# Kernel optimization log

Measured on AMD Instinct MI355X. Metric: run time of the kernel, lower is better.

The kernel has to match this reference:

```python
import jax, jax.numpy as jnp
import numpy as np

N = 100000        # nodes
E = 1600000       # edges (before self-loops)
IN_CH = 256       # input features
HEADS = 8         # conv1 heads; per-head dim also 8 (GATConv(in, heads, heads=heads))
HID = 8
NCLASS = 64
SLOPE = 0.2       # PyG leaky_relu negative slope


def _gat_conv(x, edge_index, W, att_src, att_dst, bias, heads, ch, concat):
    """PyG GATConv (eval mode): gather -> leaky_relu score -> segment softmax -> scatter."""
    n = x.shape[0]
    src, dst = edge_index[0], edge_index[1]
    h = (x @ W).reshape(n, heads, ch)                      # [N, H, C]
    a_src = jnp.einsum('nhc,hc->nh', h, att_src)           # [N, H]
    a_dst = jnp.einsum('nhc,hc->nh', h, att_dst)
    alpha = jax.nn.leaky_relu(a_src[src] + a_dst[dst], SLOPE)  # [E, H]
    # segment softmax over destination node
    amax = jax.ops.segment_max(alpha, dst, num_segments=n)     # [N, H]
    ex = jnp.exp(alpha - amax[dst])
    denom = jax.ops.segment_sum(ex, dst, num_segments=n)
    coef = ex / (denom[dst] + 1e-16)                           # [E, H]
    out = jax.ops.segment_sum(coef[:, :, None] * h[src], dst, num_segments=n)  # [N, H, C]
    if concat:
        out = out.reshape(n, heads * ch)
    else:
        out = out.mean(axis=1)
    return out + bias


def _add_self_loops(edge_index, n):
    loop = jnp.arange(n, dtype=edge_index.dtype)
    return jnp.concatenate([edge_index, jnp.stack([loop, loop])], axis=1)


def setup_inputs() -> dict:
    key = jax.random.key(0)
    ks = jax.random.split(key, 10)
    g = lambda k, shp, s: (jax.random.normal(k, shp, jnp.float32) * s)
    return {
        'x': jax.random.normal(ks[0], (N, IN_CH), jnp.float32),
        'edge_index': jax.random.randint(ks[1], (2, E), 0, N, dtype=jnp.int64),
        'W1': g(ks[2], (IN_CH, HEADS * HID), 1.0 / np.sqrt(IN_CH)),
        'att_src1': g(ks[3], (HEADS, HID), 0.3),
        'att_dst1': g(ks[4], (HEADS, HID), 0.3),
        'b1': jnp.zeros((HEADS * HID,), jnp.float32),
        'W2': g(ks[5], (HEADS * HID, NCLASS), 1.0 / np.sqrt(HEADS * HID)),
        'att_src2': g(ks[6], (1, NCLASS), 0.3),
        'att_dst2': g(ks[7], (1, NCLASS), 0.3),
        'b2': jnp.zeros((NCLASS,), jnp.float32),
    }


def reference(x, edge_index, W1, att_src1, att_dst1, b1, W2, att_src2, att_dst2, b2):
    ei = _add_self_loops(edge_index, x.shape[0])
    h = jax.nn.elu(_gat_conv(x, ei, W1, att_src1, att_dst1, b1, HEADS, HID, True))
    # dropout is a no-op in eval mode
    h = _gat_conv(h, ei, W2, att_src2, att_dst2, b2, 1, NCLASS, False)
    return jax.nn.log_softmax(h, axis=-1)
```

## Files before the change

kernel.cpp:

```cpp
#include <hip/hip_runtime.h>
#include <hip/hip_bf16.h>

#define LRELU_SLOPE 0.2f
#define CH2 6144
#define NBUK 256
#define BCAP 9728

typedef unsigned int uint;
typedef unsigned short ushort;
typedef short bt8 __attribute__((ext_vector_type(8)));
typedef float fx4 __attribute__((ext_vector_type(4)));

__device__ __forceinline__ float lrelu(float a) {
    return a > 0.f ? a : LRELU_SLOPE * a;
}
__device__ __forceinline__ ushort f2bf(float f) {
    uint u = __float_as_uint(f);
    return (ushort)((u + 0x7FFF + ((u >> 16) & 1)) >> 16);
}
__device__ __forceinline__ float bf2f(ushort h) {
    return __uint_as_float(((uint)h) << 16);
}

__global__ __launch_bounds__(256) void prep_wt(
    const float* __restrict__ W1, const float* __restrict__ W2,
    ushort* __restrict__ WT1, ushort* __restrict__ WT2)
{
    int idx = blockIdx.x * 256 + threadIdx.x;
    if (idx < 64 * 256) {
        int c = idx >> 8, k = idx & 255;
        WT1[idx] = f2bf(W1[k * 64 + c]);
    }
    int i2 = idx - 64 * 256;
    if (i2 >= 0 && i2 < 64 * 64) {
        int c = i2 >> 6, k = i2 & 63;
        WT2[i2] = f2bf(W2[k * 64 + c]);
    }
}

template<int K, bool INF32>
__global__ __launch_bounds__(256) void gemm_mfma(
    const void* __restrict__ Xv, const ushort* __restrict__ WT,
    ushort* __restrict__ OUT, int nrows)
{
    constexpr int LDW = K + 8;
    __shared__ ushort wt_l[64 * LDW];
    __shared__ ushort a_l[64 * 40];
    const int t = threadIdx.x;
    const int base = blockIdx.x * 64;

    for (int idx = t * 8; idx < 64 * K; idx += 256 * 8) {
        int r = idx / K, c = idx % K;
        *(uint4*)&wt_l[r * LDW + c] = *(const uint4*)&WT[idx];
    }
    __syncthreads();

    const int w = t >> 6, l = t & 63;
    const int frow = l & 15;
    const int kof = (l >> 4) * 8;
    fx4 acc[4] = {};

    for (int k0 = 0; k0 < K; k0 += 32) {
        if constexpr (INF32) {
            const float* X = (const float*)Xv;
            #pragma unroll
            for (int half = 0; half < 2; ++half) {
                int r = (t >> 3) + 32 * half;
                int kq = (t & 7) * 4;
                int gr = base + r;
                float4 v = make_float4(0.f, 0.f, 0.f, 0.f);
                if (gr < nrows) v = *(const float4*)(X + (size_t)gr * K + k0 + kq);
                ushort4 o;
                o.x = f2bf(v.x); o.y = f2bf(v.y); o.z = f2bf(v.z); o.w = f2bf(v.w);
                *(ushort4*)&a_l[r * 40 + kq] = o;
            }
        } else {
            const ushort* X = (const ushort*)Xv;
            int r = t >> 2;
            int kq = (t & 3) * 8;
            int gr = base + r;
            uint4 v = make_uint4(0, 0, 0, 0);
            if (gr < nrows) v = *(const uint4*)(X + (size_t)gr * K + k0 + kq);
            *(uint4*)&a_l[r * 40 + kq] = v;
        }
        __syncthreads();
        bt8 af = *(const bt8*)&a_l[(16 * w + frow) * 40 + kof];
        #pragma unroll
        for (int g = 0; g < 4; ++g) {
            bt8 bf = *(const bt8*)&wt_l[(16 * g + frow) * LDW + k0 + kof];
            acc[g] = __builtin_amdgcn_mfma_f32_16x16x32_bf16(af, bf, acc[g], 0, 0, 0);
        }
        __syncthreads();
    }

    const int orow0 = base + 16 * w + (l >> 4) * 4;
    const int ocol = l & 15;
    #pragma unroll
    for (int g = 0; g < 4; ++g) {
        #pragma unroll
        for (int r4 = 0; r4 < 4; ++r4) {
            int gr = orow0 + r4;
            if (gr < nrows) OUT[(size_t)gr * 64 + 16 * g + ocol] = f2bf(acc[g][r4]);
        }
    }
}

__global__ __launch_bounds__(256) void node_att_h8(
    const ushort* __restrict__ H, const float* __restrict__ att_s,
    const float* __restrict__ att_d,
    float* __restrict__ a_src, float* __restrict__ a_dst, int n)
{
    int node = blockIdx.x * 4 + (threadIdx.x >> 6);
    if (node >= n) return;
    int lane = threadIdx.x & 63;
    float h = bf2f(H[(size_t)node * 64 + lane]);
    float ps = h * att_s[lane];
    float pd = h * att_d[lane];
    #pragma unroll
    for (int off = 1; off < 8; off <<= 1) {
        ps += __shfl_xor(ps, off, 64);
        pd += __shfl_xor(pd, off, 64);
    }
    if ((lane & 7) == 0) {
        a_src[(size_t)node * 8 + (lane >> 3)] = ps;
        a_dst[(size_t)node * 8 + (lane >> 3)] = pd;
    }
}

__global__ __launch_bounds__(256) void node_att_h1(
    const ushort* __restrict__ H, const float* __restrict__ att_s,
    const float* __restrict__ att_d,
    float* __restrict__ a_src, float* __restrict__ a_dst, int n)
{
    int node = blockIdx.x * 4 + (threadIdx.x >> 6);
    if (node >= n) return;
    int lane = threadIdx.x & 63;
    float h = bf2f(H[(size_t)node * 64 + lane]);
    float ps = h * att_s[lane];
    float pd = h * att_d[lane];
    #pragma unroll
    for (int off = 1; off < 64; off <<= 1) {
        ps += __shfl_xor(ps, off, 64);
        pd += __shfl_xor(pd, off, 64);
    }
    if (lane == 0) { a_src[node] = ps; a_dst[node] = pd; }
}

__global__ void init_pcur(int* __restrict__ pcur)
{
    int t = threadIdx.x;
    if (t < NBUK) pcur[t] = t * BCAP;
}

__global__ __launch_bounds__(1024) void partition_pairs(
    const int* __restrict__ ei, int E_, int ET,
    int* __restrict__ pcur, uint* __restrict__ pairs)
{
    __shared__ int lcnt[NBUK], lsc[NBUK], lplace[NBUK], gpos[NBUK];
    const int t = threadIdx.x;
    const int base = blockIdx.x * CH2;
    const int total = min(CH2, ET - base);
    if (total <= 0) return;

    if (t < NBUK) lcnt[t] = 0;
    __syncthreads();

    uint pp[6]; int pk[6];
    #pragma unroll
    for (int i = 0; i < 6; ++i) {
        int idx = t + i * 1024;
        pk[i] = -1;
        if (idx < total) {
            int e = base + idx;
            int s, d;
            if (e < E_) { s = ei[e]; d = ei[E_ + e]; } else { s = d = e - E_; }
            pk[i] = d >> 9;
            pp[i] = (uint)s | ((uint)(d & 511) << 17);
            atomicAdd(&lcnt[pk[i]], 1);
        }
    }
    __syncthreads();

    if (t < NBUK) lsc[t] = lcnt[t];
    __syncthreads();
    for (int off = 1; off < NBUK; off <<= 1) {
        int add = 0;
        if (t < NBUK && t >= off) add = lsc[t - off];
        __syncthreads();
        if (t < NBUK) lsc[t] += add;
        __syncthreads();
    }
    if (t < NBUK) {
        int excl = lsc[t] - lcnt[t];
        lplace[t] = excl;
        int c = lcnt[t];
        gpos[t] = c ? (atomicAdd(&pcur[t], c) - excl) : 0;
    }
    __syncthreads();

    #pragma unroll
    for (int i = 0; i < 6; ++i) {
        if (pk[i] >= 0) {
            int slot = atomicAdd(&lplace[pk[i]], 1);
            pairs[gpos[pk[i]] + slot] = pp[i];
        }
    }
}

__global__ __launch_bounds__(256) void bucket_scan(
    const int* __restrict__ pcur, int* __restrict__ boff, int nbuk_used)
{
    __shared__ int sm[NBUK];
    int t = threadIdx.x;
    int v = (t < nbuk_used) ? (pcur[t] - t * BCAP) : 0;
    sm[t] = v; __syncthreads();
    for (int off = 1; off < NBUK; off <<= 1) {
        int add = (t >= off) ? sm[t - off] : 0;
        __syncthreads();
        sm[t] += add;
        __syncthreads();
    }
    boff[t] = sm[t] - v;
}

__global__ __launch_bounds__(1024) void phase2_build(
    const uint* __restrict__ pairs, const int* __restrict__ pcur,
    const int* __restrict__ boff,
    int* __restrict__ rp, int* __restrict__ ssrc, int n)
{
    __shared__ int hist[512], cur[512];
    const int k = blockIdx.x;
    const int t = threadIdx.x;
    const int beg = k * BCAP;
    const int cnt = pcur[k] - beg;
    const int bbase = boff[k];
    const int dbase = k << 9;

    if (t < 512) hist[t] = 0;
    __syncthreads();

    uint pp[10];
    int m = 0;
    for (int i = t; i < cnt; i += 1024) {
        uint p = pairs[beg + i];
        pp[m++] = p;
        atomicAdd(&hist[p >> 17], 1);
    }
    __syncthreads();

    int c0 = (t < 512) ? hist[t] : 0;
    for (int off = 1; off < 512; off <<= 1) {
        int add = 0;
        if (t < 512 && t >= off) add = hist[t - off];
        __syncthreads();
        if (t < 512) hist[t] += add;
        __syncthreads();
    }
    if (t < 512) {
        int node = dbase + t;
        if (node < n) rp[node] = bbase + hist[t];
        cur[t] = hist[t] - c0;
    }
    __syncthreads();

    m = 0;
    for (int i = t; i < cnt; i += 1024) {
        uint p = pp[m++];
        int j = p >> 17;
        int pos = bbase + atomicAdd(&cur[j], 1);
        ssrc[pos] = (int)(p & 0x1FFFF);
    }
}

__global__ __launch_bounds__(256) void gather_h8(
    const int* __restrict__ rp, const int* __restrict__ ssrc,
    const float* __restrict__ a_src, const float* __restrict__ a_dst,
    const ushort* __restrict__ HB, const float* __restrict__ bias,
    ushort* __restrict__ HACT, int n)
{
    int node = blockIdx.x * 8 + (threadIdx.x >> 5);
    if (node >= n) return;
    int hl = threadIdx.x & 31;
    int q = hl >> 2;
    int end = rp[node];
    int start = node ? rp[node - 1] : 0;
    float adh = a_dst[(size_t)node * 8 + q];
    float accx = 0.f, accy = 0.f, dsum = 0.f;

    for (int i0 = start; i0 < end; i0 += 32) {
        int cnt = min(32, end - i0);
        int sv = (hl < cnt) ? ssrc[i0 + hl] : 0;
        int j = 0;
        for (; j + 4 <= cnt; j += 4) {
            #pragma unroll
            for (int k = 0; k < 4; ++k) {
                int sj = __shfl(sv, j + k, 32);
                float a = a_src[(size_t)sj * 8 + q] + adh;
                a = a > 0.f ? a : LRELU_SLOPE * a;
                float e = __expf(a);
                uint hv = *(const uint*)(HB + (size_t)sj * 64 + hl * 2);
                dsum += e;
                accx += e * bf2f((ushort)(hv & 0xffff));
                accy += e * bf2f((ushort)(hv >> 16));
            }
        }
        for (; j < cnt; ++j) {
            int sj = __shfl(sv, j, 32);
            float a = a_src[(size_t)sj * 8 + q] + adh;
            a = a > 0.f ? a : LRELU_SLOPE * a;
            float e = __expf(a);
            uint hv = *(const uint*)(HB + (size_t)sj * 64 + hl * 2);
            dsum += e;
            accx += e * bf2f((ushort)(hv & 0xffff));
            accy += e * bf2f((ushort)(hv >> 16));
        }
    }
    float inv = 1.f / (dsum + 1e-16f);
    float2 bb = *(const float2*)(bias + hl * 2);
    float vx = accx * inv + bb.x;
    float vy = accy * inv + bb.y;
    vx = vx > 0.f ? vx : expm1f(vx);
    vy = vy > 0.f ? vy : expm1f(vy);
    uint pv = (uint)f2bf(vx) | ((uint)f2bf(vy) << 16);
    *(uint*)(HACT + (size_t)node * 64 + hl * 2) = pv;
}

__global__ __launch_bounds__(256) void gather_h1_lsm(
    const int* __restrict__ rp, const int* __restrict__ ssrc,
    const float* __restrict__ a_src, const float* __restrict__ a_dst,
    const ushort* __restrict__ HB, const float* __restrict__ bias,
    float* __restrict__ OUT, int n)
{
    int node = blockIdx.x * 8 + (threadIdx.x >> 5);
    if (node >= n) return;
    int hl = threadIdx.x & 31;
    int end = rp[node];
    int start = node ? rp[node - 1] : 0;
    float ad = a_dst[node];
    float accx = 0.f, accy = 0.f, dsum = 0.f;

    for (int i0 = start; i0 < end; i0 += 32) {
        int cnt = min(32, end - i0);
        int sv = (hl < cnt) ? ssrc[i0 + hl] : 0;
        int j = 0;
        for (; j + 4 <= cnt; j += 4) {
            #pragma unroll
            for (int k = 0; k < 4; ++k) {
                int sj = __shfl(sv, j + k, 32);
                float a = a_src[sj] + ad;
                a = a > 0.f ? a : LRELU_SLOPE * a;
                float e = __expf(a);
                uint hv = *(const uint*)(HB + (size_t)sj * 64 + hl * 2);
                dsum += e;
                accx += e * bf2f((ushort)(hv & 0xffff));
                accy += e * bf2f((ushort)(hv >> 16));
            }
        }
        for (; j < cnt; ++j) {
            int sj = __shfl(sv, j, 32);
            float a = a_src[sj] + ad;
            a = a > 0.f ? a : LRELU_SLOPE * a;
            float e = __expf(a);
            uint hv = *(const uint*)(HB + (size_t)sj * 64 + hl * 2);
            dsum += e;
            accx += e * bf2f((ushort)(hv & 0xffff));
            accy += e * bf2f((ushort)(hv >> 16));
        }
    }
    float inv = 1.f / (dsum + 1e-16f);
    float2 bb = *(const float2*)(bias + hl * 2);
    float vx = accx * inv + bb.x;
    float vy = accy * inv + bb.y;

    float m = fmaxf(vx, vy);
    #pragma unroll
    for (int off = 1; off < 32; off <<= 1) m = fmaxf(m, __shfl_xor(m, off, 32));
    float s = __expf(vx - m) + __expf(vy - m);
    #pragma unroll
    for (int off = 1; off < 32; off <<= 1) s += __shfl_xor(s, off, 32);
    float lse = m + __logf(s);
    *(float2*)(OUT + (size_t)node * 64 + hl * 2) = make_float2(vx - lse, vy - lse);
}

extern "C" void kernel_launch(void* const* d_in, const int* in_sizes, int n_in,
                              void* d_out, int out_size, void* d_ws, size_t ws_size,
                              hipStream_t stream)
{
    const float* x    = (const float*)d_in[0];
    const int*   ei   = (const int*)d_in[1];
    const float* W1   = (const float*)d_in[2];
    const float* as1w = (const float*)d_in[3];
    const float* ad1w = (const float*)d_in[4];
    const float* b1   = (const float*)d_in[5];
    const float* W2   = (const float*)d_in[6];
    const float* as2w = (const float*)d_in[7];
    const float* ad2w = (const float*)d_in[8];
    const float* b2   = (const float*)d_in[9];
    float* out = (float*)d_out;

    const int n  = in_sizes[0] / 256;
    const int E_ = in_sizes[1] / 2;
    const int ET = E_ + n;
    const int NBUKU = (n + 511) >> 9;

    char* wsb = (char*)d_ws;
    ushort* HACT = (ushort*)wsb;
    uint*   pairs= (uint*)wsb;
    ushort* HB   = HACT + (size_t)n * 64;
    float*  a_s1 = (float*)(HB + (size_t)n * 64);
    float*  a_d1 = a_s1 + (size_t)n * 8;
    float*  a_s2 = a_d1 + (size_t)n * 8;
    float*  a_d2 = a_s2 + n;
    int*    rp   = (int*)(a_d2 + n);
    int*    pcur = rp + n;
    int*    boff = pcur + NBUK;
    int*    ssrc = boff + NBUK;
    ushort* WT1  = (ushort*)(ssrc + ET);
    ushort* WT2  = WT1 + 64 * 256;

    const int gemm_grid = (n + 63) / 64;
    const int natt_grid = (n + 3) / 4;
    const int gath_grid = (n + 7) / 8;
    const int part_grid = (ET + CH2 - 1) / CH2;

    prep_wt<<<80, 256, 0, stream>>>(W1, W2, WT1, WT2);
    init_pcur<<<1, NBUK, 0, stream>>>(pcur);
    partition_pairs<<<part_grid, 1024, 0, stream>>>(ei, E_, ET, pcur, pairs);
    bucket_scan<<<1, NBUK, 0, stream>>>(pcur, boff, NBUKU);
    phase2_build<<<NBUKU, 1024, 0, stream>>>(pairs, pcur, boff, rp, ssrc, n);

    gemm_mfma<256, true><<<gemm_grid, 256, 0, stream>>>(x, WT1, HB, n);
    node_att_h8<<<natt_grid, 256, 0, stream>>>(HB, as1w, ad1w, a_s1, a_d1, n);
    gather_h8<<<gath_grid, 256, 0, stream>>>(rp, ssrc, a_s1, a_d1, HB, b1, HACT, n);

    gemm_mfma<64, false><<<gemm_grid, 256, 0, stream>>>(HACT, WT2, HB, n);
    node_att_h1<<<natt_grid, 256, 0, stream>>>(HB, as2w, ad2w, a_s2, a_d2, n);
    gather_h1_lsm<<<gath_grid, 256, 0, stream>>>(rp, ssrc, a_s2, a_d2, HB, b2, out, n);
}
```

Measured before the change: 198.1 us.

## Gather with 8 lanes per node using 16-byte vector loads; drop register cache in build

Both gather kernels now give each destination node 8 lanes instead of 32. Each lane loads 16 bytes (8 bf16 channels) per edge and processes the edges in fixed batches of 8, masking the tail. The log-softmax reduction shrinks to an 8-lane shuffle plus in-register work. This is meant to cut shuffle and instruction overhead per edge and widen memory transactions, but gives fewer lanes per edge and some wasted masked work on low-degree nodes. Separately, phase2_build re-reads pairs from global memory instead of caching them in a register array, which lowers register pressure at the cost of a second read.

```diff
diff --git a/kernel.cpp b/kernel.cpp
--- a/kernel.cpp
+++ b/kernel.cpp
@@ -239,13 +239,8 @@
     if (t < 512) hist[t] = 0;
     __syncthreads();
 
-    uint pp[10];
-    int m = 0;
-    for (int i = t; i < cnt; i += 1024) {
-        uint p = pairs[beg + i];
-        pp[m++] = p;
-        atomicAdd(&hist[p >> 17], 1);
-    }
+    for (int i = t; i < cnt; i += 1024)
+        atomicAdd(&hist[pairs[beg + i] >> 17], 1);
     __syncthreads();
 
     int c0 = (t < 512) ? hist[t] : 0;
@@ -263,9 +258,8 @@
     }
     __syncthreads();
 
-    m = 0;
     for (int i = t; i < cnt; i += 1024) {
-        uint p = pp[m++];
+        uint p = pairs[beg + i];
         int j = p >> 17;
         int pos = bbase + atomicAdd(&cur[j], 1);
         ssrc[pos] = (int)(p & 0x1FFFF);
@@ -278,51 +272,53 @@
     const ushort* __restrict__ HB, const float* __restrict__ bias,
     ushort* __restrict__ HACT, int n)
 {
-    int node = blockIdx.x * 8 + (threadIdx.x >> 5);
+    int node = blockIdx.x * 32 + (threadIdx.x >> 3);
     if (node >= n) return;
-    int hl = threadIdx.x & 31;
-    int q = hl >> 2;
+    int ol = threadIdx.x & 7;
     int end = rp[node];
     int start = node ? rp[node - 1] : 0;
-    float adh = a_dst[(size_t)node * 8 + q];
-    float accx = 0.f, accy = 0.f, dsum = 0.f;
-
-    for (int i0 = start; i0 < end; i0 += 32) {
-        int cnt = min(32, end - i0);
-        int sv = (hl < cnt) ? ssrc[i0 + hl] : 0;
-        int j = 0;
-        for (; j + 4 <= cnt; j += 4) {
-            #pragma unroll
-            for (int k = 0; k < 4; ++k) {
-                int sj = __shfl(sv, j + k, 32);
-                float a = a_src[(size_t)sj * 8 + q] + adh;
-                a = a > 0.f ? a : LRELU_SLOPE * a;
-                float e = __expf(a);
-                uint hv = *(const uint*)(HB + (size_t)sj * 64 + hl * 2);
-                dsum += e;
-                accx += e * bf2f((ushort)(hv & 0xffff));
-                accy += e * bf2f((ushort)(hv >> 16));
-            }
-        }
-        for (; j < cnt; ++j) {
-            int sj = __shfl(sv, j, 32);
-            float a = a_src[(size_t)sj * 8 + q] + adh;
+    float adh = a_dst[(size_t)node * 8 + ol];
+    float acc[8] = {};
+    float dsum = 0.f;
+
+    for (int i0 = start; i0 < end; i0 += 8) {
+        int cnt = min(8, end - i0);
+        int sv = (ol < cnt) ? ssrc[i0 + ol] : 0;
+        #pragma unroll
+        for (int j = 0; j < 8; ++j) {
+            int sj = __shfl(sv, j, 8);
+            float a = a_src[(size_t)sj * 8 + ol] + adh;
             a = a > 0.f ? a : LRELU_SLOPE * a;
             float e = __expf(a);
-            uint hv = *(const uint*)(HB + (size_t)sj * 64 + hl * 2);
+            e = (j < cnt) ? e : 0.f;
             dsum += e;
-            accx += e * bf2f((ushort)(hv & 0xffff));
-            accy += e * bf2f((ushort)(hv >> 16));
+            uint4 hv = *(const uint4*)(HB + (size_t)sj * 64 + ol * 8);
+            acc[0] += e * bf2f((ushort)(hv.x & 0xffff));
+            acc[1] += e * bf2f((ushort)(hv.x >> 16));
+            acc[2] += e * bf2f((ushort)(hv.y & 0xffff));
+            acc[3] += e * bf2f((ushort)(hv.y >> 16));
+            acc[4] += e * bf2f((ushort)(hv.z & 0xffff));
+            acc[5] += e * bf2f((ushort)(hv.z >> 16));
+            acc[6] += e * bf2f((ushort)(hv.w & 0xffff));
+            acc[7] += e * bf2f((ushort)(hv.w >> 16));
         }
     }
     float inv = 1.f / (dsum + 1e-16f);
-    float2 bb = *(const float2*)(bias + hl * 2);
-    float vx = accx * inv + bb.x;
-    float vy = accy * inv + bb.y;
-    vx = vx > 0.f ? vx : expm1f(vx);
-    vy = vy > 0.f ? vy : expm1f(vy);
-    uint pv = (uint)f2bf(vx) | ((uint)f2bf(vy) << 16);
-    *(uint*)(HACT + (size_t)node * 64 + hl * 2) = pv;
+    float4 b0 = *(const float4*)(bias + ol * 8);
+    float4 b1 = *(const float4*)(bias + ol * 8 + 4);
+    float v[8];
+    v[0] = acc[0] * inv + b0.x; v[1] = acc[1] * inv + b0.y;
+    v[2] = acc[2] * inv + b0.z; v[3] = acc[3] * inv + b0.w;
+    v[4] = acc[4] * inv + b1.x; v[5] = acc[5] * inv + b1.y;
+    v[6] = acc[6] * inv + b1.z; v[7] = acc[7] * inv + b1.w;
+    #pragma unroll
+    for (int c = 0; c < 8; ++c) v[c] = v[c] > 0.f ? v[c] : expm1f(v[c]);
+    uint4 o;
+    o.x = (uint)f2bf(v[0]) | ((uint)f2bf(v[1]) << 16);
+    o.y = (uint)f2bf(v[2]) | ((uint)f2bf(v[3]) << 16);
+    o.z = (uint)f2bf(v[4]) | ((uint)f2bf(v[5]) << 16);
+    o.w = (uint)f2bf(v[6]) | ((uint)f2bf(v[7]) << 16);
+    *(uint4*)(HACT + (size_t)node * 64 + ol * 8) = o;
 }
 
 __global__ __launch_bounds__(256) void gather_h1_lsm(
@@ -331,55 +327,63 @@
     const ushort* __restrict__ HB, const float* __restrict__ bias,
     float* __restrict__ OUT, int n)
 {
-    int node = blockIdx.x * 8 + (threadIdx.x >> 5);
+    int node = blockIdx.x * 32 + (threadIdx.x >> 3);
     if (node >= n) return;
-    int hl = threadIdx.x & 31;
+    int ol = threadIdx.x & 7;
     int end = rp[node];
     int start = node ? rp[node - 1] : 0;
     float ad = a_dst[node];
-    float accx = 0.f, accy = 0.f, dsum = 0.f;
-
-    for (int i0 = start; i0 < end; i0 += 32) {
-        int cnt = min(32, end - i0);
-        int sv = (hl < cnt) ? ssrc[i0 + hl] : 0;
-        int j = 0;
-        for (; j + 4 <= cnt; j += 4) {
-            #pragma unroll
-            for (int k = 0; k < 4; ++k) {
-                int sj = __shfl(sv, j + k, 32);
-                float a = a_src[sj] + ad;
-                a = a > 0.f ? a : LRELU_SLOPE * a;
-                float e = __expf(a);
-                uint hv = *(const uint*)(HB + (size_t)sj * 64 + hl * 2);
-                dsum += e;
-                accx += e * bf2f((ushort)(hv & 0xffff));
-                accy += e * bf2f((ushort)(hv >> 16));
-            }
-        }
-        for (; j < cnt; ++j) {
-            int sj = __shfl(sv, j, 32);
+    float acc[8] = {};
+    float dsum = 0.f;
+
+    for (int i0 = start; i0 < end; i0 += 8) {
+        int cnt = min(8, end - i0);
+        int sv = (ol < cnt) ? ssrc[i0 + ol] : 0;
+        #pragma unroll
+        for (int j = 0; j < 8; ++j) {
+            int sj = __shfl(sv, j, 8);
             float a = a_src[sj] + ad;
             a = a > 0.f ? a : LRELU_SLOPE * a;
             float e = __expf(a);
-            uint hv = *(const uint*)(HB + (size_t)sj * 64 + hl * 2);
+            e = (j < cnt) ? e : 0.f;
             dsum += e;
-            accx += e * bf2f((ushort)(hv & 0xffff));
-            accy += e * bf2f((ushort)(hv >> 16));
+            uint4 hv = *(const uint4*)(HB + (size_t)sj * 64 + ol * 8);
+            acc[0] += e * bf2f((ushort)(hv.x & 0xffff));
+            acc[1] += e * bf2f((ushort)(hv.x >> 16));
+            acc[2] += e * bf2f((ushort)(hv.y & 0xffff));
+            acc[3] += e * bf2f((ushort)(hv.y >> 16));
+            acc[4] += e * bf2f((ushort)(hv.z & 0xffff));
+            acc[5] += e * bf2f((ushort)(hv.z >> 16));
+            acc[6] += e * bf2f((ushort)(hv.w & 0xffff));
+            acc[7] += e * bf2f((ushort)(hv.w >> 16));
         }
     }
     float inv = 1.f / (dsum + 1e-16f);
-    float2 bb = *(const float2*)(bias + hl * 2);
-    float vx = accx * inv + bb.x;
-    float vy = accy * inv + bb.y;
-
-    float m = fmaxf(vx, vy);
-    #pragma unroll
-    for (int off = 1; off < 32; off <<= 1) m = fmaxf(m, __shfl_xor(m, off, 32));
-    float s = __expf(vx - m) + __expf(vy - m);
-    #pragma unroll
-    for (int off = 1; off < 32; off <<= 1) s += __shfl_xor(s, off, 32);
+    float4 b0 = *(const float4*)(bias + ol * 8);
+    float4 b1 = *(const float4*)(bias + ol * 8 + 4);
+    float v[8];
+    v[0] = acc[0] * inv + b0.x; v[1] = acc[1] * inv + b0.y;
+    v[2] = acc[2] * inv + b0.z; v[3] = acc[3] * inv + b0.w;
+    v[4] = acc[4] * inv + b1.x; v[5] = acc[5] * inv + b1.y;
+    v[6] = acc[6] * inv + b1.z; v[7] = acc[7] * inv + b1.w;
+
+    float m = v[0];
+    #pragma unroll
+    for (int c = 1; c < 8; ++c) m = fmaxf(m, v[c]);
+    m = fmaxf(m, __shfl_xor(m, 1, 8));
+    m = fmaxf(m, __shfl_xor(m, 2, 8));
+    m = fmaxf(m, __shfl_xor(m, 4, 8));
+    float s = 0.f;
+    #pragma unroll
+    for (int c = 0; c < 8; ++c) s += __expf(v[c] - m);
+    s += __shfl_xor(s, 1, 8);
+    s += __shfl_xor(s, 2, 8);
+    s += __shfl_xor(s, 4, 8);
     float lse = m + __logf(s);
-    *(float2*)(OUT + (size_t)node * 64 + hl * 2) = make_float2(vx - lse, vy - lse);
+    float4 o0 = make_float4(v[0] - lse, v[1] - lse, v[2] - lse, v[3] - lse);
+    float4 o1 = make_float4(v[4] - lse, v[5] - lse, v[6] - lse, v[7] - lse);
+    *(float4*)(OUT + (size_t)node * 64 + ol * 8) = o0;
+    *(float4*)(OUT + (size_t)node * 64 + ol * 8 + 4) = o1;
 }
 
 extern "C" void kernel_launch(void* const* d_in, const int* in_sizes, int n_in,
@@ -420,7 +424,7 @@
 
     const int gemm_grid = (n + 63) / 64;
     const int natt_grid = (n + 3) / 4;
-    const int gath_grid = (n + 7) / 8;
+    const int gath_grid = (n + 31) / 32;
     const int part_grid = (ET + CH2 - 1) / CH2;
 
     prep_wt<<<80, 256, 0, stream>>>(W1, W2, WT1, WT2);
```

Measured after the change: 189.6 us. 1.04x faster.
